# Kernel tuning notes

Measured on AMD Instinct MI355X. Metric: run time of the kernel, lower is better.

Reference implementation:

```python
import jax, jax.numpy as jnp
import numpy as np

B, T, C = 4, 2048, 1024
E = 8           # num_experts
H = 4 * C       # expert hidden dim


def setup_inputs() -> dict:
    key = jax.random.key(0)
    ks = jax.random.split(key, 4)
    s = 0.02
    return {
        "x":  jax.random.normal(ks[0], (B, T, C), jnp.float32),
        "Wr": jax.random.normal(ks[1], (C, E), jnp.float32) * s,
        "br": jnp.zeros((E,), jnp.float32),
        "W1": jax.random.normal(ks[2], (E, C, H), jnp.float32) * s,
        "b1": jnp.zeros((E, H), jnp.float32),
        "W2": jax.random.normal(ks[3], (E, H, C), jnp.float32) * s,
        "b2": jnp.zeros((E, C), jnp.float32),
    }


def reference(x, Wr, br, W1, b1, W2, b2):
    Bs, Ts, Cs = x.shape
    n_exp = W1.shape[0]
    xf = x.reshape(-1, Cs)                      # [N, C]
    logits = xf @ Wr + br                       # [N, E]
    gates = jax.nn.softmax(logits, axis=-1)
    probs = gates.max(axis=-1)                  # top-1 gate value [N]
    idx = gates.argmax(axis=-1)                 # expert assignment [N]

    # Masked-dense dispatch: each expert processes all tokens, mask zeroes
    # non-assigned tokens (same math as gather/MLP/scatter in the original;
    # a fused grouped-GEMM kernel would avoid the redundant FLOPs).
    out = jnp.zeros_like(xf)
    for e in range(n_exp):
        h = jax.nn.gelu(xf @ W1[e] + b1[e], approximate=False)  # [N, H]
        y = h @ W2[e] + b2[e]                                   # [N, C]
        g = jnp.where(idx == e, probs, 0.0)                     # [N]
        out = out + g[:, None] * y

    # load-balance aux loss (counts are non-differentiable, as in torch no_grad)
    counts = jnp.bincount(idx, length=n_exp).astype(jnp.float32)
    frac = counts / jnp.maximum(counts.sum(), 1.0)
    uniform = 1.0 / n_exp
    aux = jnp.mean((frac - uniform) ** 2)

    return out.reshape(Bs, Ts, Cs), aux
```

## Files before the change

### kernel.cpp

```cpp
#include <hip/hip_runtime.h>
#include <hip/hip_bf16.h>
#include <stdint.h>

#define N_TOK 8192
#define C_DIM 1024
#define E_NUM 8
#define H_DIM 4096
#define ROWS_PAD 9216
#define HBLK 32

typedef __attribute__((ext_vector_type(8))) short bf16x8;
typedef __attribute__((ext_vector_type(4))) float f32x4;

static __device__ __forceinline__ unsigned short f2bf(float f) {
    union { float f; unsigned u; } v; v.f = f;
    unsigned r = (v.u + 0x7FFFu + ((v.u >> 16) & 1u)) >> 16;
    return (unsigned short)r;
}

static __device__ __forceinline__ void load_lds16(const unsigned short* g, unsigned short* l) {
    __builtin_amdgcn_global_load_lds(
        (const __attribute__((address_space(1))) unsigned int*)g,
        (__attribute__((address_space(3))) unsigned int*)l, 16, 0, 0);
}

#define TP_STRIDE 258
__global__ __launch_bounds__(256) void transpose_w(const float* __restrict__ in,
                                                   unsigned short* __restrict__ out,
                                                   int K, int N) {
    __shared__ unsigned short tile[64 * TP_STRIDE];
    int e  = blockIdx.z;
    int n0 = blockIdx.x * 64;
    int k0 = blockIdx.y * 256;
    int t = threadIdx.x;
    int lane = t & 63;
    int w = t >> 6;

    const float* ip = in + (size_t)e * K * N + (size_t)k0 * N + n0 + lane;
    unsigned short* lrow = &tile[lane * TP_STRIDE];
#pragma unroll 8
    for (int i = 0; i < 64; i++) {
        int k = w * 64 + i;
        lrow[k] = f2bf(ip[(size_t)k * N]);
    }
    __syncthreads();

    unsigned short* op = out + (size_t)e * N * K + (size_t)n0 * K + k0;
    for (int j = 0; j < 16; j++) {
        int n = w * 16 + j;
        const unsigned* src = (const unsigned*)&tile[n * TP_STRIDE];
        unsigned* dst = (unsigned*)&op[(size_t)n * K];
        dst[lane]      = src[lane];
        dst[lane + 64] = src[lane + 64];
    }
}

__global__ void router_kernel(const float* __restrict__ x, const float* __restrict__ Wr,
                              const float* __restrict__ br,
                              float* __restrict__ probs, int* __restrict__ eidx) {
    int n = blockIdx.x * 4 + (threadIdx.x >> 6);
    int lane = threadIdx.x & 63;
    const float* xr = x + (size_t)n * C_DIM;
    double acc[E_NUM];
#pragma unroll
    for (int e = 0; e < E_NUM; e++) acc[e] = 0.0;
    for (int i = 0; i < 16; i++) {
        int c = i * 64 + lane;
        float xv = xr[c];
        const float4* wr = (const float4*)(Wr + c * E_NUM);
        float4 w0 = wr[0], w1 = wr[1];
        acc[0] += (double)xv * w0.x; acc[1] += (double)xv * w0.y;
        acc[2] += (double)xv * w0.z; acc[3] += (double)xv * w0.w;
        acc[4] += (double)xv * w1.x; acc[5] += (double)xv * w1.y;
        acc[6] += (double)xv * w1.z; acc[7] += (double)xv * w1.w;
    }
#pragma unroll
    for (int e = 0; e < E_NUM; e++) {
#pragma unroll
        for (int o = 32; o > 0; o >>= 1) acc[e] += __shfl_xor(acc[e], o, 64);
    }
    if (lane == 0) {
        float l[E_NUM];
        for (int e = 0; e < E_NUM; e++) l[e] = (float)acc[e] + br[e];
        int arg = 0; float m = l[0];
        for (int e = 1; e < E_NUM; e++) if (l[e] > m) { m = l[e]; arg = e; }
        float s = 0.f;
        for (int e = 0; e < E_NUM; e++) s += expf(l[e] - m);
        probs[n] = 1.0f / s;
        eidx[n] = arg;
    }
}

__global__ void hist_kernel(const int* __restrict__ eidx, int* __restrict__ blk_cnt) {
    __shared__ int lh[E_NUM];
    int t = threadIdx.x, b = blockIdx.x;
    if (t < E_NUM) lh[t] = 0;
    __syncthreads();
    atomicAdd(&lh[eidx[b * 256 + t]], 1);
    __syncthreads();
    if (t < E_NUM) blk_cnt[b * E_NUM + t] = lh[t];
}

__global__ void finalize_kernel(const int* __restrict__ blk_cnt, int* __restrict__ cnt,
                                int* __restrict__ seg, int* __restrict__ blockbase,
                                float* __restrict__ aux_out) {
    int e = threadIdx.x;
    int c[HBLK];
    int tot = 0;
    if (e < E_NUM) {
#pragma unroll
        for (int b = 0; b < HBLK; b++) { c[b] = blk_cnt[b * E_NUM + e]; tot += c[b]; }
    }
    int pad = ((tot + 127) >> 7) << 7;
    int sg = 0;
#pragma unroll
    for (int j = 0; j < E_NUM; j++) {
        int pj = __shfl(pad, j, 64);
        if (j < e) sg += pj;
    }
    if (e < E_NUM) {
        cnt[e] = tot;
        seg[e] = sg;
        int run = sg;
#pragma unroll
        for (int b = 0; b < HBLK; b++) { blockbase[b * E_NUM + e] = run; run += c[b]; }
        float fr = (float)tot / (float)N_TOK - 1.0f / (float)E_NUM;
        float s = fr * fr;
#pragma unroll
        for (int o = 4; o > 0; o >>= 1) s += __shfl_xor(s, o, 64);
        if (e == 0) aux_out[0] = s / (float)E_NUM;
    }
}

__global__ void gatherpos_kernel(const float* __restrict__ probs, const int* __restrict__ eidx,
                                 const int* __restrict__ blockbase, int* __restrict__ tok_row,
                                 int* __restrict__ inv_row, float* __restrict__ rowprob) {
    __shared__ int lh[E_NUM];
    int t = threadIdx.x, b = blockIdx.x;
    if (t < E_NUM) lh[t] = 0;
    __syncthreads();
    int n = b * 256 + t;
    int e = eidx[n];
    int lrank = atomicAdd(&lh[e], 1);
    int row = blockbase[b * E_NUM + e] + lrank;
    tok_row[n] = row;
    inv_row[row] = n;
    rowprob[row] = probs[n];
}

__global__ void copy_kernel(const float* __restrict__ x, const int* __restrict__ tok_row,
                            unsigned short* __restrict__ xg) {
    int n = blockIdx.x * 4 + (threadIdx.x >> 6);
    int lane = threadIdx.x & 63;
    int row = tok_row[n];
    const float4* xr = (const float4*)(x + (size_t)n * C_DIM);
    uint2* xgr = (uint2*)(xg + (size_t)row * C_DIM);
#pragma unroll
    for (int i = 0; i < 4; i++) {
        float4 v = xr[i * 64 + lane];
        uint2 p;
        p.x = (unsigned)f2bf(v.x) | ((unsigned)f2bf(v.y) << 16);
        p.y = (unsigned)f2bf(v.z) | ((unsigned)f2bf(v.w) << 16);
        xgr[i * 64 + lane] = p;
    }
}

template <int KDIM, int NDIM, int EPI>
__global__ __launch_bounds__(256) void moe_gemm(
    const unsigned short* __restrict__ Ag, const unsigned short* __restrict__ Bt,
    const float* __restrict__ bias, unsigned short* __restrict__ hg,
    float* __restrict__ out, const int* __restrict__ cnt, const int* __restrict__ seg,
    const int* __restrict__ inv_row, const float* __restrict__ rowprob) {
    int mt = blockIdx.y;
    int e;
    for (e = 0; e < E_NUM; e++) {
        int te = (cnt[e] + 127) >> 7;
        if (mt < te) break;
        mt -= te;
    }
    if (e >= E_NUM) return;
    int row0 = seg[e] + mt * 128;
    int col0 = blockIdx.x * 128;

    __shared__ unsigned short As[128 * 32];
    __shared__ unsigned short Bs[128 * 32];

    const unsigned short* Ab = Ag + (size_t)row0 * KDIM;
    const unsigned short* Bb = Bt + (size_t)e * NDIM * KDIM + (size_t)col0 * KDIM;

    int tid = threadIdx.x;
    int lane = tid & 63;
    int wv = tid >> 6;
    int wr = (wv >> 1) * 64, wc = (wv & 1) * 64;

    f32x4 acc[4][4] = {};

    int srow = lane >> 2;
    int scol = (lane & 3) * 8;

    for (int kk = 0; kk < KDIM; kk += 32) {
#pragma unroll
        for (int r = 0; r < 2; r++) {
            int chunk = wv + 4 * r;
            int rowa = 16 * chunk + srow;
            load_lds16(Ab + (size_t)rowa * KDIM + kk + scol, &As[16 * chunk * 32]);
            load_lds16(Bb + (size_t)rowa * KDIM + kk + scol, &Bs[16 * chunk * 32]);
        }
        __syncthreads();
        bf16x8 af[4], bfr[4];
        int fr = lane & 15, fq = (lane >> 4) * 8;
#pragma unroll
        for (int i = 0; i < 4; i++) {
            af[i]  = *(const bf16x8*)&As[(wr + i * 16 + fr) * 32 + fq];
            bfr[i] = *(const bf16x8*)&Bs[(wc + i * 16 + fr) * 32 + fq];
        }
#pragma unroll
        for (int i = 0; i < 4; i++)
#pragma unroll
            for (int j = 0; j < 4; j++)
                acc[i][j] = __builtin_amdgcn_mfma_f32_16x16x32_bf16(af[i], bfr[j], acc[i][j], 0, 0, 0);
        __syncthreads();
    }

    int cl = lane & 15, rq = (lane >> 4) * 4;
#pragma unroll
    for (int i = 0; i < 4; i++) {
#pragma unroll
        for (int j = 0; j < 4; j++) {
            int gcol = col0 + wc + j * 16 + cl;
            float b = bias[e * NDIM + gcol];
#pragma unroll
            for (int r = 0; r < 4; r++) {
                int grow = row0 + wr + i * 16 + rq + r;
                float v = acc[i][j][r] + b;
                if (EPI == 1) {
                    v = 0.5f * v * (1.0f + erff(v * 0.70710678118654752f));
                    hg[(size_t)grow * NDIM + gcol] = f2bf(v);
                } else {
                    int token = inv_row[grow];
                    if (token >= 0) out[(size_t)token * NDIM + gcol] = rowprob[grow] * v;
                }
            }
        }
    }
}

extern "C" void kernel_launch(void* const* d_in, const int* in_sizes, int n_in,
                              void* d_out, int out_size, void* d_ws, size_t ws_size,
                              hipStream_t stream) {
    const float* x  = (const float*)d_in[0];
    const float* Wr = (const float*)d_in[1];
    const float* br = (const float*)d_in[2];
    const float* W1 = (const float*)d_in[3];
    const float* b1 = (const float*)d_in[4];
    const float* W2 = (const float*)d_in[5];
    const float* b2 = (const float*)d_in[6];
    float* out = (float*)d_out;

    char* ws = (char*)d_ws;
    unsigned short* W1t = (unsigned short*)ws;
    unsigned short* W2t = (unsigned short*)(ws + (64ull << 20));
    unsigned short* xg  = (unsigned short*)(ws + (128ull << 20));
    unsigned short* hg  = (unsigned short*)(ws + (128ull << 20) + 18874368ull);
    char* small = ws + (128ull << 20) + 18874368ull + 75497472ull;
    float* probs     = (float*)small;
    int*   eidx      = (int*)(small + 32768);
    float* rowprob   = (float*)(small + 65536);
    int*   inv_row   = (int*)(small + 65536 + 36864);
    int*   tok_row   = (int*)(small + 65536 + 73728);
    int*   blk_cnt   = (int*)(small + 65536 + 73728 + 32768);
    int*   blockbase = blk_cnt + HBLK * E_NUM;
    int*   cnt       = blockbase + HBLK * E_NUM;
    int*   seg       = cnt + 8;

    hipMemsetAsync(xg, 0, (size_t)ROWS_PAD * C_DIM * 2, stream);
    hipMemsetAsync(inv_row, 0xFF, ROWS_PAD * 4, stream);

    transpose_w<<<dim3(H_DIM / 64, C_DIM / 256, E_NUM), 256, 0, stream>>>(W1, W1t, C_DIM, H_DIM);
    transpose_w<<<dim3(C_DIM / 64, H_DIM / 256, E_NUM), 256, 0, stream>>>(W2, W2t, H_DIM, C_DIM);

    router_kernel<<<N_TOK / 4, 256, 0, stream>>>(x, Wr, br, probs, eidx);
    hist_kernel<<<HBLK, 256, 0, stream>>>(eidx, blk_cnt);
    finalize_kernel<<<1, 64, 0, stream>>>(blk_cnt, cnt, seg, blockbase,
                                          out + (size_t)N_TOK * C_DIM);
    gatherpos_kernel<<<HBLK, 256, 0, stream>>>(probs, eidx, blockbase, tok_row, inv_row, rowprob);
    copy_kernel<<<N_TOK / 4, 256, 0, stream>>>(x, tok_row, xg);

    moe_gemm<C_DIM, H_DIM, 1><<<dim3(H_DIM / 128, 72), 256, 0, stream>>>(
        xg, W1t, b1, hg, nullptr, cnt, seg, inv_row, rowprob);
    moe_gemm<H_DIM, C_DIM, 2><<<dim3(C_DIM / 128, 72), 256, 0, stream>>>(
        hg, W2t, b2, nullptr, out, cnt, seg, inv_row, rowprob);
}
```

Measured before the change: 634.5 us.

## Rewrite grouped MoE GEMM with 256x256 tiles, swizzled LDS and pipelined phases

The grouped expert GEMM moves from 128x128 tiles with a K-step of 32 and 4 waves to 256x256 tiles with a K-step of 64 and 8 waves. Expert segments are padded to 256 rows. The kernel double-buffers A and B halves in XOR-swizzled LDS and splits each K-step into four phases that interleave global-to-LDS staging with MFMA work, using explicit barriers, vmcnt waits and setprio. The aim is more reuse per loaded byte, fewer LDS bank conflicts and latency hidden behind MFMA. In exchange it pads more rows per expert, launches fewer blocks (possibly poor CU occupancy on the N=1024 second GEMM), and uses far more LDS and registers per block.

Measured after the change: 616.8 us. -2.8%, faster.

```diff
diff --git a/kernel.cpp b/kernel.cpp
--- a/kernel.cpp
+++ b/kernel.cpp
@@ -6,8 +6,9 @@
 #define C_DIM 1024
 #define E_NUM 8
 #define H_DIM 4096
-#define ROWS_PAD 9216
+#define ROWS_PAD 10240
 #define HBLK 32
+#define MT_MAX 40
 
 typedef __attribute__((ext_vector_type(8))) short bf16x8;
 typedef __attribute__((ext_vector_type(4))) float f32x4;
@@ -22,6 +23,12 @@
     __builtin_amdgcn_global_load_lds(
         (const __attribute__((address_space(1))) unsigned int*)g,
         (__attribute__((address_space(3))) unsigned int*)l, 16, 0, 0);
+}
+
+static __device__ __forceinline__ bf16x8 rfrag(const unsigned short* hb, int r, int ks, int hi) {
+    int byte = r * 128 + ks * 64 + hi * 16;
+    byte ^= (r & 7) << 4;
+    return *(const bf16x8*)((const char*)hb + byte);
 }
 
 #define TP_STRIDE 258
@@ -111,7 +118,7 @@
 #pragma unroll
         for (int b = 0; b < HBLK; b++) { c[b] = blk_cnt[b * E_NUM + e]; tot += c[b]; }
     }
-    int pad = ((tot + 127) >> 7) << 7;
+    int pad = ((tot + 255) >> 8) << 8;
     int sg = 0;
 #pragma unroll
     for (int j = 0; j < E_NUM; j++) {
@@ -165,8 +172,54 @@
     }
 }
 
+#define STAGE(d, ab, h, G, kt) do {                                            \
+    _Pragma("unroll")                                                          \
+    for (int i_ = 0; i_ < 2; i_++) {                                           \
+        int idx_ = i_ * 512 + tid;                                             \
+        int row_ = idx_ >> 3;                                                  \
+        int us_ = (idx_ & 7) ^ (row_ & 7);                                     \
+        load_lds16((G) + (size_t)((h) * 128 + row_) * KDIM + (kt) * 64 + us_ * 8, \
+                   &lds[d][ab][h][(i_ * 512 + (tid & ~63)) * 8]);              \
+    } } while (0)
+
+#define PHASE(D, MH, NH, LA, LB, STAGE_STMT, WAIT_STMT) do {                   \
+    if (LA) {                                                                  \
+        _Pragma("unroll")                                                      \
+        for (int i_ = 0; i_ < 4; i_++) {                                       \
+            int r_ = wm * 64 + i_ * 16 + (lane & 15);                          \
+            af[i_][0] = rfrag(&lds[D][0][MH][0], r_, 0, hi);                   \
+            af[i_][1] = rfrag(&lds[D][0][MH][0], r_, 1, hi);                   \
+        }                                                                      \
+    }                                                                          \
+    if (LB) {                                                                  \
+        _Pragma("unroll")                                                      \
+        for (int j_ = 0; j_ < 2; j_++) {                                       \
+            int c_ = wn * 32 + j_ * 16 + (lane & 15);                          \
+            bf[NH][j_][0] = rfrag(&lds[D][1][NH][0], c_, 0, hi);               \
+            bf[NH][j_][1] = rfrag(&lds[D][1][NH][0], c_, 1, hi);               \
+        }                                                                      \
+    }                                                                          \
+    STAGE_STMT;                                                                \
+    __builtin_amdgcn_s_barrier();                                              \
+    asm volatile("s_waitcnt lgkmcnt(0)" ::: "memory");                         \
+    __builtin_amdgcn_s_setprio(1);                                             \
+    _Pragma("unroll")                                                          \
+    for (int i_ = 0; i_ < 4; i_++) {                                           \
+        _Pragma("unroll")                                                      \
+        for (int j_ = 0; j_ < 2; j_++) {                                       \
+            acc[MH][i_][NH][j_] = __builtin_amdgcn_mfma_f32_16x16x32_bf16(     \
+                af[i_][0], bf[NH][j_][0], acc[MH][i_][NH][j_], 0, 0, 0);       \
+            acc[MH][i_][NH][j_] = __builtin_amdgcn_mfma_f32_16x16x32_bf16(     \
+                af[i_][1], bf[NH][j_][1], acc[MH][i_][NH][j_], 0, 0, 0);       \
+        }                                                                      \
+    }                                                                          \
+    __builtin_amdgcn_s_setprio(0);                                             \
+    WAIT_STMT;                                                                 \
+    __builtin_amdgcn_s_barrier();                                              \
+} while (0)
+
 template <int KDIM, int NDIM, int EPI>
-__global__ __launch_bounds__(256) void moe_gemm(
+__global__ __launch_bounds__(512) void moe_gemm(
     const unsigned short* __restrict__ Ag, const unsigned short* __restrict__ Bt,
     const float* __restrict__ bias, unsigned short* __restrict__ hg,
     float* __restrict__ out, const int* __restrict__ cnt, const int* __restrict__ seg,
@@ -174,16 +227,15 @@
     int mt = blockIdx.y;
     int e;
     for (e = 0; e < E_NUM; e++) {
-        int te = (cnt[e] + 127) >> 7;
+        int te = (cnt[e] + 255) >> 8;
         if (mt < te) break;
         mt -= te;
     }
     if (e >= E_NUM) return;
-    int row0 = seg[e] + mt * 128;
-    int col0 = blockIdx.x * 128;
-
-    __shared__ unsigned short As[128 * 32];
-    __shared__ unsigned short Bs[128 * 32];
+    int row0 = seg[e] + mt * 256;
+    int col0 = blockIdx.x * 256;
+
+    __shared__ unsigned short lds[2][2][2][128 * 64];
 
     const unsigned short* Ab = Ag + (size_t)row0 * KDIM;
     const unsigned short* Bb = Bt + (size_t)e * NDIM * KDIM + (size_t)col0 * KDIM;
@@ -191,55 +243,58 @@
     int tid = threadIdx.x;
     int lane = tid & 63;
     int wv = tid >> 6;
-    int wr = (wv >> 1) * 64, wc = (wv & 1) * 64;
-
-    f32x4 acc[4][4] = {};
-
-    int srow = lane >> 2;
-    int scol = (lane & 3) * 8;
-
-    for (int kk = 0; kk < KDIM; kk += 32) {
-#pragma unroll
-        for (int r = 0; r < 2; r++) {
-            int chunk = wv + 4 * r;
-            int rowa = 16 * chunk + srow;
-            load_lds16(Ab + (size_t)rowa * KDIM + kk + scol, &As[16 * chunk * 32]);
-            load_lds16(Bb + (size_t)rowa * KDIM + kk + scol, &Bs[16 * chunk * 32]);
-        }
-        __syncthreads();
-        bf16x8 af[4], bfr[4];
-        int fr = lane & 15, fq = (lane >> 4) * 8;
-#pragma unroll
-        for (int i = 0; i < 4; i++) {
-            af[i]  = *(const bf16x8*)&As[(wr + i * 16 + fr) * 32 + fq];
-            bfr[i] = *(const bf16x8*)&Bs[(wc + i * 16 + fr) * 32 + fq];
-        }
-#pragma unroll
-        for (int i = 0; i < 4; i++)
-#pragma unroll
-            for (int j = 0; j < 4; j++)
-                acc[i][j] = __builtin_amdgcn_mfma_f32_16x16x32_bf16(af[i], bfr[j], acc[i][j], 0, 0, 0);
-        __syncthreads();
-    }
-
-    int cl = lane & 15, rq = (lane >> 4) * 4;
-#pragma unroll
-    for (int i = 0; i < 4; i++) {
-#pragma unroll
-        for (int j = 0; j < 4; j++) {
-            int gcol = col0 + wc + j * 16 + cl;
-            float b = bias[e * NDIM + gcol];
-#pragma unroll
-            for (int r = 0; r < 4; r++) {
-                int grow = row0 + wr + i * 16 + rq + r;
-                float v = acc[i][j][r] + b;
-                if (EPI == 1) {
-                    v = 0.5f * v * (1.0f + erff(v * 0.70710678118654752f));
-                    hg[(size_t)grow * NDIM + gcol] = f2bf(v);
-                } else {
-                    int token = inv_row[grow];
-                    if (token >= 0) out[(size_t)token * NDIM + gcol] = rowprob[grow] * v;
-                }
+    int wm = wv >> 2;
+    int wn = wv & 3;
+    int hi = lane >> 4;
+
+    f32x4 acc[2][4][2][2] = {};
+    bf16x8 af[4][2], bf[2][2][2];
+
+    const int NT = KDIM / 64;
+
+    STAGE(0, 0, 0, Ab, 0);
+    STAGE(0, 0, 1, Ab, 0);
+    STAGE(0, 1, 0, Bb, 0);
+    STAGE(0, 1, 1, Bb, 0);
+    STAGE(1, 0, 0, Ab, 1);
+    STAGE(1, 1, 1, Bb, 1);
+    STAGE(1, 0, 1, Ab, 1);
+    asm volatile("s_waitcnt vmcnt(6)" ::: "memory");
+    __builtin_amdgcn_s_barrier();
+
+    for (int t = 0; t < NT; t++) {
+        int d = t & 1, dn = d ^ 1;
+        bool s1 = (t + 1 < NT), s2 = (t + 2 < NT);
+        PHASE(d, 0, 0, 1, 1, { if (s1) STAGE(dn, 1, 0, Bb, t + 1); }, {});
+        PHASE(d, 0, 1, 0, 1, { if (s2) STAGE(d, 0, 0, Ab, t + 2); }, {});
+        PHASE(d, 1, 0, 1, 0, { if (s2) STAGE(d, 1, 1, Bb, t + 2); }, {});
+        PHASE(d, 1, 1, 0, 0, { if (s2) STAGE(d, 0, 1, Ab, t + 2); },
+              { if (s2)      { asm volatile("s_waitcnt vmcnt(6)" ::: "memory"); }
+                else if (s1) { asm volatile("s_waitcnt vmcnt(0)" ::: "memory"); } });
+    }
+
+    int cl = lane & 15, rq = (lane >> 4) << 2;
+#pragma unroll
+    for (int MH = 0; MH < 2; MH++)
+#pragma unroll
+    for (int i = 0; i < 4; i++)
+#pragma unroll
+    for (int NH = 0; NH < 2; NH++)
+#pragma unroll
+    for (int j = 0; j < 2; j++) {
+        int gcol = col0 + NH * 128 + wn * 32 + j * 16 + cl;
+        float b = bias[e * NDIM + gcol];
+        int growb = row0 + MH * 128 + wm * 64 + i * 16 + rq;
+#pragma unroll
+        for (int r = 0; r < 4; r++) {
+            int grow = growb + r;
+            float v = acc[MH][i][NH][j][r] + b;
+            if (EPI == 1) {
+                v = 0.5f * v * (1.0f + erff(v * 0.70710678118654752f));
+                hg[(size_t)grow * NDIM + gcol] = f2bf(v);
+            } else {
+                int token = inv_row[grow];
+                if (token >= 0) out[(size_t)token * NDIM + gcol] = rowprob[grow] * v;
             }
         }
     }
@@ -259,16 +314,16 @@
 
     char* ws = (char*)d_ws;
     unsigned short* W1t = (unsigned short*)ws;
-    unsigned short* W2t = (unsigned short*)(ws + (64ull << 20));
-    unsigned short* xg  = (unsigned short*)(ws + (128ull << 20));
-    unsigned short* hg  = (unsigned short*)(ws + (128ull << 20) + 18874368ull);
-    char* small = ws + (128ull << 20) + 18874368ull + 75497472ull;
+    unsigned short* W2t = (unsigned short*)(ws + 67108864ull);
+    unsigned short* xg  = (unsigned short*)(ws + 134217728ull);
+    unsigned short* hg  = (unsigned short*)(ws + 155189248ull);
+    char* small = ws + 239075328ull;
     float* probs     = (float*)small;
     int*   eidx      = (int*)(small + 32768);
     float* rowprob   = (float*)(small + 65536);
-    int*   inv_row   = (int*)(small + 65536 + 36864);
-    int*   tok_row   = (int*)(small + 65536 + 73728);
-    int*   blk_cnt   = (int*)(small + 65536 + 73728 + 32768);
+    int*   inv_row   = (int*)(small + 106496);
+    int*   tok_row   = (int*)(small + 147456);
+    int*   blk_cnt   = (int*)(small + 180224);
     int*   blockbase = blk_cnt + HBLK * E_NUM;
     int*   cnt       = blockbase + HBLK * E_NUM;
     int*   seg       = cnt + 8;
@@ -286,8 +341,8 @@
     gatherpos_kernel<<<HBLK, 256, 0, stream>>>(probs, eidx, blockbase, tok_row, inv_row, rowprob);
     copy_kernel<<<N_TOK / 4, 256, 0, stream>>>(x, tok_row, xg);
 
-    moe_gemm<C_DIM, H_DIM, 1><<<dim3(H_DIM / 128, 72), 256, 0, stream>>>(
+    moe_gemm<C_DIM, H_DIM, 1><<<dim3(H_DIM / 256, MT_MAX), 512, 0, stream>>>(
         xg, W1t, b1, hg, nullptr, cnt, seg, inv_row, rowprob);
-    moe_gemm<H_DIM, C_DIM, 2><<<dim3(C_DIM / 128, 72), 256, 0, stream>>>(
+    moe_gemm<H_DIM, C_DIM, 2><<<dim3(C_DIM / 256, MT_MAX), 512, 0, stream>>>(
         hg, W2t, b2, nullptr, out, cnt, seg, inv_row, rowprob);
 }
```
